# Optimization experiments

Measured on AMD Instinct MI355X. Metric: run time of the kernel, lower is better.

The kernel has to match this reference:

```python
import jax, jax.numpy as jnp
import numpy as np
import math

K_NEIGH = 8
STRIDE = 4
EPS = 1e-8

def _gather(feats, idx):
    # feats (B,N,D), idx (B,M,K) -> (B,M,K,D)
    return jax.vmap(lambda f, i: f[i])(feats, idx)

def _knn_idx(q, p, k):
    # squared-distance KNN, indices sorted by ascending distance
    d2 = (q * q).sum(-1)[:, :, None] + (p * p).sum(-1)[:, None, :] - 2.0 * jnp.einsum('bmd,bnd->bmn', q, p)
    _, idx = jax.lax.top_k(-d2, k)
    return idx

def _fps(pos, k):
    # farthest point sampling, start at index 0 (pytorch3d default)
    B, N, _ = pos.shape
    start = jnp.zeros((B,), dtype=jnp.int32)
    mind = jnp.full((B, N), jnp.inf, dtype=pos.dtype)
    def body(carry, _):
        mind, last = carry
        lp = jax.vmap(lambda p, i: p[i])(pos, last)  # (B,3)
        d = ((pos - lp[:, None, :]) ** 2).sum(-1)
        mind = jnp.minimum(mind, d)
        nxt = jnp.argmax(mind, axis=-1).astype(jnp.int32)
        return (mind, nxt), nxt
    _, nxts = jax.lax.scan(body, (mind, start), None, length=k - 1)
    idx = jnp.concatenate([start[None], nxts], axis=0).swapaxes(0, 1)  # (B,k)
    fp = jax.vmap(lambda p, i: p[i])(pos, idx)
    return fp

def _gelu(t):
    return jax.nn.gelu(t, approximate=False)

def setup_inputs() -> dict:
    key = jax.random.key(0)
    N, B, D = 8192, 2, 128
    ks = jax.random.split(key, 16)
    w = lambda k, i, o: 0.02 * jax.random.normal(k, (i, o), dtype=jnp.float32)
    return {
        'x': jax.random.normal(ks[0], (N, B, D), dtype=jnp.float32),
        'p_pos': jax.random.uniform(ks[1], (B, N, 3), dtype=jnp.float32),
        'Wq': w(ks[2], D, D), 'bq': jnp.zeros((D,), jnp.float32),
        'Wk': w(ks[3], D, D), 'bk': jnp.zeros((D,), jnp.float32),
        'Wv': w(ks[4], D, D), 'bv': jnp.zeros((D,), jnp.float32),
        'Wpe1': w(ks[5], 3, D), 'bpe1': jnp.zeros((D,), jnp.float32),
        'Wpe2': w(ks[6], D, D), 'bpe2': jnp.zeros((D,), jnp.float32),
        'Wg': w(ks[7], D, D), 'bg': jnp.zeros((D,), jnp.float32),
        'Wo': w(ks[8], D, D), 'bo': jnp.zeros((D,), jnp.float32),
        'scale': jnp.ones((D,), jnp.float32),
        'Wf1': w(ks[9], D, 4 * D), 'bf1': jnp.zeros((4 * D,), jnp.float32),
        'Wf2': w(ks[10], 4 * D, 2 * D), 'bf2': jnp.zeros((2 * D,), jnp.float32),
        'Wpool': w(ks[11], 3 + 2 * D, 2 * D),
    }

def reference(x, p_pos, Wq, bq, Wk, bk, Wv, bv, Wpe1, bpe1, Wpe2, bpe2, Wg, bg, Wo, bo, scale, Wf1, bf1, Wf2, bf2, Wpool):
    D = x.shape[-1]
    # --- PointAttention ---
    xt = jnp.swapaxes(x, 0, 1)                      # (B,N,D)
    q = xt @ Wq + bq
    k = xt @ Wk + bk
    v = xt @ Wv + bv
    idx = _knn_idx(p_pos, p_pos, K_NEIGH)           # (B,N,K)
    knn_pos = _gather(p_pos, idx)                   # (B,N,K,3)
    k_knn = _gather(k, idx)
    v_knn = _gather(v, idx)
    pe = _gelu((p_pos[:, :, None, :] - knn_pos) @ Wpe1 + bpe1) @ Wpe2 + bpe2
    attn = (q[:, :, None, :] - k_knn + pe) @ Wg + bg
    attn = jax.nn.softmax(attn / math.sqrt(D), axis=-1)  # softmax over feature dim, as in source
    res = jnp.einsum('bmnf,bmnf->bmf', attn, v_knn + pe)
    res = res @ Wo + bo
    x = x + jnp.swapaxes(res, 0, 1)                 # (N,B,D)
    # --- RMSNorm ---
    rms = jnp.sqrt((x * x).sum(-1, keepdims=True)) / math.sqrt(D)
    x = scale * (x / (rms + EPS))
    # --- FFN ---
    x = _gelu(x @ Wf1 + bf1) @ Wf2 + bf2            # (N,B,2D)
    # --- PointPool ---
    xt2 = jnp.swapaxes(x, 0, 1)                     # (B,N,2D)
    n_out = p_pos.shape[1] // STRIDE
    fp_pos = jax.lax.stop_gradient(_fps(p_pos, n_out))    # (B,n_out,3)
    kidx = jax.lax.stop_gradient(_knn_idx(fp_pos, p_pos, K_NEIGH))
    knn_x = _gather(xt2, kidx)                      # (B,n_out,K,2D)
    h = jnp.concatenate([jnp.broadcast_to(fp_pos[:, :, None, :], knn_x.shape[:3] + (3,)), knn_x], axis=-1)
    h = h @ Wpool
    h = jnp.where(h >= 0, h, 0.01 * h)              # LeakyReLU(0.01)
    h = h.max(axis=-2)                              # (B,n_out,2D)
    return jnp.swapaxes(h, 0, 1), fp_pos
```

## Files before the change

### kernel.cpp

```cpp
#include <hip/hip_runtime.h>
#include <math.h>

#define N_PTS   8192
#define BATCH   2
#define DIM     128
#define NOUT    2048
#define FPOFF   1048576
#define SLICE_MAX 1400

__device__ __forceinline__ float gelu_f(float v) {
  return 0.5f * v * (1.0f + erff(v * 0.70710678118654752440f));
}

__device__ __forceinline__ void knn_insert(float (&dist)[8], int (&idq)[8],
                                           float d2, int ci) {
  if (d2 < dist[7]) {
    float dd = d2;
#pragma unroll
    for (int j = 0; j < 8; ++j) {
      bool cc = dd < dist[j];
      float td = dist[j]; int ti = idq[j];
      dist[j] = cc ? dd : td; idq[j] = cc ? ci : ti;
      dd = cc ? td : dd; ci = cc ? ti : ci;
    }
  }
}

__device__ __forceinline__ void fps_slice(
    const float* __restrict__ P, float* __restrict__ MWS, float* __restrict__ LPWS,
    float* __restrict__ FPWS, float* __restrict__ OUTFP,
    int b, int t0, int t1)
{
  __builtin_amdgcn_s_setprio(3);
  __shared__ unsigned long long wkeys[2][8];
  __shared__ float hist[SLICE_MAX * 3];
  const int tid = threadIdx.x;
  const int wv = tid >> 6;
  const float* __restrict__ Pb = P + (long)b * N_PTS * 3;
  float px[16], py[16], pz[16], mind[16];
#pragma unroll
  for (int s = 0; s < 16; ++s) {
    int i = s * 512 + tid;
    px[s] = Pb[i * 3 + 0];
    py[s] = Pb[i * 3 + 1];
    pz[s] = Pb[i * 3 + 2];
  }
  float lx, ly, lz;
  if (t0 == 0) {
#pragma unroll
    for (int s = 0; s < 16; ++s) mind[s] = INFINITY;
    lx = Pb[0]; ly = Pb[1]; lz = Pb[2];
    if (tid == 0) { hist[0] = lx; hist[1] = ly; hist[2] = lz; }
  } else {
#pragma unroll
    for (int s = 0; s < 16; ++s) mind[s] = MWS[b * N_PTS + s * 512 + tid];
    lx = LPWS[b * 4 + 0]; ly = LPWS[b * 4 + 1]; lz = LPWS[b * 4 + 2];
  }
  const int tstart = (t0 == 0) ? 1 : t0;
  for (int t = tstart; t < t1; ++t) {
    const int par = t & 1;
    float bv = -INFINITY; int bs = 0;
#pragma unroll
    for (int s = 0; s < 16; ++s) {
      float dx = __fsub_rn(px[s], lx);
      float dy = __fsub_rn(py[s], ly);
      float dz = __fsub_rn(pz[s], lz);
      float d = __fadd_rn(__fadd_rn(__fmul_rn(dx, dx), __fmul_rn(dy, dy)), __fmul_rn(dz, dz));
      float mm = fminf(mind[s], d);
      mind[s] = mm;
      bool c = mm > bv;
      bv = c ? mm : bv; bs = c ? s : bs;
    }
    unsigned long long key =
        ((unsigned long long)__float_as_uint(bv) << 32) |
        (unsigned int)~(unsigned int)(bs * 512 + tid);
#pragma unroll
    for (int off = 1; off <= 32; off <<= 1) {
      unsigned long long o = __shfl_xor(key, off);
      key = (o > key) ? o : key;
    }
    if ((tid & 63) == 0) wkeys[par][wv] = key;
    __syncthreads();
    unsigned long long wk = wkeys[par][0];
#pragma unroll
    for (int u = 1; u < 8; ++u) {
      unsigned long long o = wkeys[par][u];
      wk = (o > wk) ? o : wk;
    }
    const int idx = (int)(~(unsigned int)wk);
    lx = Pb[idx * 3 + 0];
    ly = Pb[idx * 3 + 1];
    lz = Pb[idx * 3 + 2];
    if (tid == 0) {
      int h = (t - t0) * 3;
      hist[h + 0] = lx; hist[h + 1] = ly; hist[h + 2] = lz;
    }
  }
#pragma unroll
  for (int s = 0; s < 16; ++s) MWS[b * N_PTS + s * 512 + tid] = mind[s];
  if (tid == 0) { LPWS[b * 4 + 0] = lx; LPWS[b * 4 + 1] = ly; LPWS[b * 4 + 2] = lz; }
  __syncthreads();
  const int cnt = (t1 - t0) * 3;
  const long base = ((long)b * NOUT + t0) * 3;
  for (int i = tid; i < cnt; i += 512) {
    float v2 = hist[i];
    FPWS[base + i] = v2;
    OUTFP[FPOFF + base + i] = v2;
  }
  __builtin_amdgcn_s_setprio(0);
}

__device__ __forceinline__ void knn2p_body(
    const float* __restrict__ Q, const float* __restrict__ Pp,
    float* __restrict__ PD, int* __restrict__ PI, int qg, int r)
{
  __shared__ float4 shp[512];
  const int b = qg >> 2;
  const int m = (qg & 3) * 512 + threadIdx.x;
  const float qx = Q[(b * NOUT + m) * 3 + 0];
  const float qy = Q[(b * NOUT + m) * 3 + 1];
  const float qz = Q[(b * NOUT + m) * 3 + 2];
  const float sqq = __fadd_rn(__fadd_rn(__fmul_rn(qx, qx), __fmul_rn(qy, qy)), __fmul_rn(qz, qz));
  float dist[8]; int idq[8];
#pragma unroll
  for (int j = 0; j < 8; ++j) { dist[j] = INFINITY; idq[j] = 0; }
  const int cb = r * 1024;
  for (int tt = 0; tt < 1024; tt += 512) {
    __syncthreads();
    {
      int l = threadIdx.x;
      float x = Pp[(b * N_PTS + cb + tt + l) * 3 + 0];
      float y = Pp[(b * N_PTS + cb + tt + l) * 3 + 1];
      float z = Pp[(b * N_PTS + cb + tt + l) * 3 + 2];
      float s = __fadd_rn(__fadd_rn(__fmul_rn(x, x), __fmul_rn(y, y)), __fmul_rn(z, z));
      shp[l] = make_float4(x, y, z, s);
    }
    __syncthreads();
    for (int c = 0; c < 512; c += 4) {
      float4 p0 = shp[c + 0];
      float4 p1 = shp[c + 1];
      float4 p2 = shp[c + 2];
      float4 p3 = shp[c + 3];
      float d0 = __fsub_rn(__fadd_rn(sqq, p0.w), __fmul_rn(2.0f,
                 __fadd_rn(__fadd_rn(__fmul_rn(qx, p0.x), __fmul_rn(qy, p0.y)), __fmul_rn(qz, p0.z))));
      float d1 = __fsub_rn(__fadd_rn(sqq, p1.w), __fmul_rn(2.0f,
                 __fadd_rn(__fadd_rn(__fmul_rn(qx, p1.x), __fmul_rn(qy, p1.y)), __fmul_rn(qz, p1.z))));
      float d2 = __fsub_rn(__fadd_rn(sqq, p2.w), __fmul_rn(2.0f,
                 __fadd_rn(__fadd_rn(__fmul_rn(qx, p2.x), __fmul_rn(qy, p2.y)), __fmul_rn(qz, p2.z))));
      float d3 = __fsub_rn(__fadd_rn(sqq, p3.w), __fmul_rn(2.0f,
                 __fadd_rn(__fadd_rn(__fmul_rn(qx, p3.x), __fmul_rn(qy, p3.y)), __fmul_rn(qz, p3.z))));
      float mn = fminf(fminf(d0, d1), fminf(d2, d3));
      if (mn < dist[7]) {
        knn_insert(dist, idq, d0, cb + tt + c + 0);
        knn_insert(dist, idq, d1, cb + tt + c + 1);
        knn_insert(dist, idq, d2, cb + tt + c + 2);
        knn_insert(dist, idq, d3, cb + tt + c + 3);
      }
    }
  }
  const long ob = ((long)(b * NOUT + m) * 8 + r) * 8;
#pragma unroll
  for (int j = 0; j < 8; ++j) { PD[ob + j] = dist[j]; PI[ob + j] = idq[j]; }
}

__global__ __launch_bounds__(512) void fps_fin(
    const float* __restrict__ P, float* __restrict__ MWS, float* __restrict__ LPWS,
    float* __restrict__ FPWS, float* __restrict__ OUTFP,
    float* __restrict__ PD2, int* __restrict__ PI2, int t0, int t1)
{
  if ((int)blockIdx.x < 2) {
    fps_slice(P, MWS, LPWS, FPWS, OUTFP, (int)blockIdx.x, t0, t1);
    return;
  }
  const int wid = (int)blockIdx.x - 2;
  const int qidx = wid >> 3;
  const int r = wid & 7;
  const int qg = qidx * 4;
  knn2p_body(FPWS, P, PD2, PI2, qg, r);
}

__global__ __launch_bounds__(512) void knn2pb_k(
    const float* __restrict__ Q, const float* __restrict__ Pp,
    float* __restrict__ PD, int* __restrict__ PI)
{
  const int qidx = (int)blockIdx.x >> 3;
  const int r = (int)blockIdx.x & 7;
  const int qg = (qidx < 3) ? (qidx + 1) : (qidx + 2);
  knn2p_body(Q, Pp, PD, PI, qg, r);
}

__global__ __launch_bounds__(512) void gemm2_k(
    const float* __restrict__ A, const float* __restrict__ W,
    const float* __restrict__ bias, float* __restrict__ OUT,
    const float* __restrict__ resid,
    int nbx, int N, int K, int a_mode, int o_mode, int act,
    const float* __restrict__ P, float* __restrict__ MWS, float* __restrict__ LPWS,
    float* __restrict__ FPWS, float* __restrict__ OUTFP, int t0, int t1)
{
  if ((int)blockIdx.x < 2) {
    fps_slice(P, MWS, LPWS, FPWS, OUTFP, (int)blockIdx.x, t0, t1);
    return;
  }
  const int wid = (int)blockIdx.x - 2;
  __shared__ float As[2][16][132];
  __shared__ float Ws2[2][16][132];
  const int team = threadIdx.x >> 8;
  const int tid = threadIdx.x & 255;
  const int tx = tid & 15, ty = tid >> 4;
  const int bx = wid % nbx;
  const int byy = (wid / nbx) * 2 + team;
  float acc[8][8];
#pragma unroll
  for (int i = 0; i < 8; ++i)
#pragma unroll
    for (int j = 0; j < 8; ++j) acc[i][j] = 0.f;

  for (int k0 = 0; k0 < K; k0 += 16) {
#pragma unroll
    for (int rep = 0; rep < 2; ++rep) {
      int qq = tid + rep * 256;
      int m = qq >> 2, kq = qq & 3;
      int r = byy * 128 + m;
      int arow = (a_mode == 1) ? ((r & 8191) * 2 + (r >> 13)) : r;
      const float4 av = *(const float4*)(A + (long)arow * K + k0 + kq * 4);
      As[team][kq * 4 + 0][m] = av.x; As[team][kq * 4 + 1][m] = av.y;
      As[team][kq * 4 + 2][m] = av.z; As[team][kq * 4 + 3][m] = av.w;
      int kw = qq >> 5, nq = qq & 31;
      const float4 wv = *(const float4*)(W + (long)(k0 + kw) * N + bx * 128 + nq * 4);
      *(float4*)&Ws2[team][kw][nq * 4] = wv;
    }
    __syncthreads();
#pragma unroll
    for (int kk = 0; kk < 16; ++kk) {
      float4 a0 = *(const float4*)&As[team][kk][ty * 8];
      float4 a1 = *(const float4*)&As[team][kk][ty * 8 + 4];
      float4 w0 = *(const float4*)&Ws2[team][kk][tx * 4];
      float4 w1 = *(const float4*)&Ws2[team][kk][64 + tx * 4];
      float am[8] = {a0.x, a0.y, a0.z, a0.w, a1.x, a1.y, a1.z, a1.w};
      float wn[8] = {w0.x, w0.y, w0.z, w0.w, w1.x, w1.y, w1.z, w1.w};
#pragma unroll
      for (int i = 0; i < 8; ++i)
#pragma unroll
        for (int j = 0; j < 8; ++j) acc[i][j] += am[i] * wn[j];
    }
    __syncthreads();
  }
  const int c0 = bx * 128 + tx * 4;
  const int c1 = c0 + 64;
  float4 ba = *(const float4*)(bias + c0);
  float4 bb = *(const float4*)(bias + c1);
#pragma unroll
  for (int i = 0; i < 8; ++i) {
    int r = byy * 128 + ty * 8 + i;
    int orow = (o_mode == 1) ? ((r & 8191) * 2 + (r >> 13))
             : (o_mode == 2) ? ((r & 1) * 8192 + (r >> 1)) : r;
    float o[8] = {acc[i][0] + ba.x, acc[i][1] + ba.y, acc[i][2] + ba.z, acc[i][3] + ba.w,
                  acc[i][4] + bb.x, acc[i][5] + bb.y, acc[i][6] + bb.z, acc[i][7] + bb.w};
    if (act == 1) {
#pragma unroll
      for (int j = 0; j < 8; ++j) o[j] = gelu_f(o[j]);
    }
    if (resid) {
      float4 r0 = *(const float4*)(resid + (long)orow * N + c0);
      float4 r1 = *(const float4*)(resid + (long)orow * N + c1);
      o[0] += r0.x; o[1] += r0.y; o[2] += r0.z; o[3] += r0.w;
      o[4] += r1.x; o[5] += r1.y; o[6] += r1.z; o[7] += r1.w;
    }
    *(float4*)(OUT + (long)orow * N + c0) = make_float4(o[0], o[1], o[2], o[3]);
    *(float4*)(OUT + (long)orow * N + c1) = make_float4(o[4], o[5], o[6], o[7]);
  }
}

__global__ __launch_bounds__(512) void gemmqkv_k(
    const float* __restrict__ A,
    const float* __restrict__ Wq, const float* __restrict__ bq, float* __restrict__ Oq,
    const float* __restrict__ Wk, const float* __restrict__ bk, float* __restrict__ Ok,
    const float* __restrict__ Wv, const float* __restrict__ bv, float* __restrict__ Ov,
    const float* __restrict__ P, float* __restrict__ MWS, float* __restrict__ LPWS,
    float* __restrict__ FPWS, float* __restrict__ OUTFP, int t0, int t1)
{
  if ((int)blockIdx.x < 2) {
    fps_slice(P, MWS, LPWS, FPWS, OUTFP, (int)blockIdx.x, t0, t1);
    return;
  }
  const int wid = (int)blockIdx.x - 2;
  const int sel = wid >> 6;
  const float* W = (sel == 0) ? Wq : (sel == 1) ? Wk : Wv;
  const float* bias = (sel == 0) ? bq : (sel == 1) ? bk : bv;
  float* OUT = (sel == 0) ? Oq : (sel == 1) ? Ok : Ov;
  __shared__ float As[2][16][132];
  __shared__ float Ws2[2][16][132];
  const int team = threadIdx.x >> 8;
  const int tid = threadIdx.x & 255;
  const int tx = tid & 15, ty = tid >> 4;
  const int byy = (wid & 63) * 2 + team;
  float acc[8][8];
#pragma unroll
  for (int i = 0; i < 8; ++i)
#pragma unroll
    for (int j = 0; j < 8; ++j) acc[i][j] = 0.f;

  for (int k0 = 0; k0 < 128; k0 += 16) {
#pragma unroll
    for (int rep = 0; rep < 2; ++rep) {
      int qq = tid + rep * 256;
      int m = qq >> 2, kq = qq & 3;
      int r = byy * 128 + m;
      int arow = (r & 8191) * 2 + (r >> 13);
      const float4 av = *(const float4*)(A + (long)arow * 128 + k0 + kq * 4);
      As[team][kq * 4 + 0][m] = av.x; As[team][kq * 4 + 1][m] = av.y;
      As[team][kq * 4 + 2][m] = av.z; As[team][kq * 4 + 3][m] = av.w;
      int kw = qq >> 5, nq = qq & 31;
      const float4 wv = *(const float4*)(W + (long)(k0 + kw) * 128 + nq * 4);
      *(float4*)&Ws2[team][kw][nq * 4] = wv;
    }
    __syncthreads();
#pragma unroll
    for (int kk = 0; kk < 16; ++kk) {
      float4 a0 = *(const float4*)&As[team][kk][ty * 8];
      float4 a1 = *(const float4*)&As[team][kk][ty * 8 + 4];
      float4 w0 = *(const float4*)&Ws2[team][kk][tx * 4];
      float4 w1 = *(const float4*)&Ws2[team][kk][64 + tx * 4];
      float am[8] = {a0.x, a0.y, a0.z, a0.w, a1.x, a1.y, a1.z, a1.w};
      float wn[8] = {w0.x, w0.y, w0.z, w0.w, w1.x, w1.y, w1.z, w1.w};
#pragma unroll
      for (int i = 0; i < 8; ++i)
#pragma unroll
        for (int j = 0; j < 8; ++j) acc[i][j] += am[i] * wn[j];
    }
    __syncthreads();
  }
  const int c0 = tx * 4;
  const int c1 = c0 + 64;
  float4 ba = *(const float4*)(bias + c0);
  float4 bb = *(const float4*)(bias + c1);
#pragma unroll
  for (int i = 0; i < 8; ++i) {
    int orow = byy * 128 + ty * 8 + i;
    float o[8] = {acc[i][0] + ba.x, acc[i][1] + ba.y, acc[i][2] + ba.z, acc[i][3] + ba.w,
                  acc[i][4] + bb.x, acc[i][5] + bb.y, acc[i][6] + bb.z, acc[i][7] + bb.w};
    *(float4*)(OUT + (long)orow * 128 + c0) = make_float4(o[0], o[1], o[2], o[3]);
    *(float4*)(OUT + (long)orow * 128 + c1) = make_float4(o[4], o[5], o[6], o[7]);
  }
}

__global__ __launch_bounds__(512) void knn1p_k(
    const float* __restrict__ Pp, float* __restrict__ PD, int* __restrict__ PI,
    const float* __restrict__ P, float* __restrict__ MWS, float* __restrict__ LPWS,
    float* __restrict__ FPWS, float* __restrict__ OUTFP, int t0, int t1)
{
  if ((int)blockIdx.x < 2) {
    fps_slice(P, MWS, LPWS, FPWS, OUTFP, (int)blockIdx.x, t0, t1);
    return;
  }
  const int wid = (int)blockIdx.x - 2;
  const int qg = wid >> 2;
  const int r = wid & 3;
  const int b = qg >> 4;
  const int m = (qg & 15) * 512 + threadIdx.x;
  __shared__ float4 shp[512];
  const float qx = Pp[(b * N_PTS + m) * 3 + 0];
  const float qy = Pp[(b * N_PTS + m) * 3 + 1];
  const float qz = Pp[(b * N_PTS + m) * 3 + 2];
  const float sqq = __fadd_rn(__fadd_rn(__fmul_rn(qx, qx), __fmul_rn(qy, qy)), __fmul_rn(qz, qz));
  float dist[8]; int idq[8];
#pragma unroll
  for (int j = 0; j < 8; ++j) { dist[j] = INFINITY; idq[j] = 0; }
  const int cb = r * 2048;
  for (int tt = 0; tt < 2048; tt += 512) {
    __syncthreads();
    {
      int l = threadIdx.x;
      float x = Pp[(b * N_PTS + cb + tt + l) * 3 + 0];
      float y = Pp[(b * N_PTS + cb + tt + l) * 3 + 1];
      float z = Pp[(b * N_PTS + cb + tt + l) * 3 + 2];
      float s = __fadd_rn(__fadd_rn(__fmul_rn(x, x), __fmul_rn(y, y)), __fmul_rn(z, z));
      shp[l] = make_float4(x, y, z, s);
    }
    __syncthreads();
    for (int c = 0; c < 512; c += 4) {
      float4 p0 = shp[c + 0];
      float4 p1 = shp[c + 1];
      float4 p2 = shp[c + 2];
      float4 p3 = shp[c + 3];
      float d0 = __fsub_rn(__fadd_rn(sqq, p0.w), __fmul_rn(2.0f,
                 __fadd_rn(__fadd_rn(__fmul_rn(qx, p0.x), __fmul_rn(qy, p0.y)), __fmul_rn(qz, p0.z))));
      float d1 = __fsub_rn(__fadd_rn(sqq, p1.w), __fmul_rn(2.0f,
                 __fadd_rn(__fadd_rn(__fmul_rn(qx, p1.x), __fmul_rn(qy, p1.y)), __fmul_rn(qz, p1.z))));
      float d2 = __fsub_rn(__fadd_rn(sqq, p2.w), __fmul_rn(2.0f,
                 __fadd_rn(__fadd_rn(__fmul_rn(qx, p2.x), __fmul_rn(qy, p2.y)), __fmul_rn(qz, p2.z))));
      float d3 = __fsub_rn(__fadd_rn(sqq, p3.w), __fmul_rn(2.0f,
                 __fadd_rn(__fadd_rn(__fmul_rn(qx, p3.x), __fmul_rn(qy, p3.y)), __fmul_rn(qz, p3.z))));
      float mn = fminf(fminf(d0, d1), fminf(d2, d3));
      if (mn < dist[7]) {
        knn_insert(dist, idq, d0, cb + tt + c + 0);
        knn_insert(dist, idq, d1, cb + tt + c + 1);
        knn_insert(dist, idq, d2, cb + tt + c + 2);
        knn_insert(dist, idq, d3, cb + tt + c + 3);
      }
    }
  }
  const long ob = ((long)(b * N_PTS + m) * 4 + r) * 8;
#pragma unroll
  for (int j = 0; j < 8; ++j) { PD[ob + j] = dist[j]; PI[ob + j] = idq[j]; }
}

__global__ __launch_bounds__(512) void attn_k(
    const float* __restrict__ Qb, const float* __restrict__ Kb, const float* __restrict__ Vb,
    const float* __restrict__ Pp,
    const float* __restrict__ PD1, const int* __restrict__ PI1,
    const float* __restrict__ Wpe1, const float* __restrict__ bpe1,
    const float* __restrict__ Wpe2, const float* __restrict__ bpe2,
    const float* __restrict__ Wg, const float* __restrict__ bg,
    float* __restrict__ RES,
    const float* __restrict__ P, float* __restrict__ MWS, float* __restrict__ LPWS,
    float* __restrict__ FPWS, float* __restrict__ OUTFP, int t0, int t1)
{
  if ((int)blockIdx.x < 2) {
    fps_slice(P, MWS, LPWS, FPWS, OUTFP, (int)blockIdx.x, t0, t1);
    return;
  }
  __shared__ float sbuf[8][1024];
  const int tid = threadIdx.x;
  const int w = tid >> 6, lane = tid & 63;
  const int g = ((int)blockIdx.x - 2) * 8 + w;
  const int b = g >> 13, n = g & 8191;
  const int j0 = lane * 2;
  float* sb = sbuf[w];
  const float2 qv = *(const float2*)(Qb + (long)g * 128 + j0);
  float mdist[8]; int nb[8];
#pragma unroll
  for (int j = 0; j < 8; ++j) { mdist[j] = INFINITY; nb[j] = 0; }
#pragma unroll
  for (int r = 0; r < 4; ++r) {
    const long ob = ((long)g * 4 + r) * 8;
#pragma unroll
    for (int j = 0; j < 8; ++j) knn_insert(mdist, nb, PD1[ob + j], PI1[ob + j]);
  }
  const float p0 = Pp[(b * N_PTS + n) * 3 + 0];
  const float p1 = Pp[(b * N_PTS + n) * 3 + 1];
  const float p2 = Pp[(b * N_PTS + n) * 3 + 2];
  const float2 w1a = *(const float2*)(Wpe1 + j0);
  const float2 w1b = *(const float2*)(Wpe1 + 128 + j0);
  const float2 w1c = *(const float2*)(Wpe1 + 256 + j0);
  const float2 b1 = *(const float2*)(bpe1 + j0);
#pragma unroll
  for (int kk = 0; kk < 8; ++kk) {
    const float* pn = Pp + (long)(b * N_PTS + nb[kk]) * 3;
    float r0 = p0 - pn[0], r1 = p1 - pn[1], r2 = p2 - pn[2];
    float h0 = r0 * w1a.x + r1 * w1b.x + r2 * w1c.x + b1.x;
    float h1 = r0 * w1a.y + r1 * w1b.y + r2 * w1c.y + b1.y;
    sb[kk * 128 + j0]     = gelu_f(h0);
    sb[kk * 128 + j0 + 1] = gelu_f(h1);
  }
  __syncthreads();
  float2 pe[8];
#pragma unroll
  for (int kk = 0; kk < 8; ++kk) pe[kk] = make_float2(0.f, 0.f);
  for (int i = 0; i < 128; i += 2) {
    float2 wa = *(const float2*)(Wpe2 + (long)i * 128 + j0);
    float2 wb = *(const float2*)(Wpe2 + (long)(i + 1) * 128 + j0);
#pragma unroll
    for (int kk = 0; kk < 8; ++kk) {
      float2 hh = *(const float2*)&sb[kk * 128 + i];
      pe[kk].x += hh.x * wa.x + hh.y * wb.x;
      pe[kk].y += hh.x * wa.y + hh.y * wb.y;
    }
  }
  const float2 b2v = *(const float2*)(bpe2 + j0);
  __syncthreads();
#pragma unroll
  for (int kk = 0; kk < 8; ++kk) {
    pe[kk].x += b2v.x; pe[kk].y += b2v.y;
    const float2 kv = *(const float2*)(Kb + (long)(b * N_PTS + nb[kk]) * 128 + j0);
    sb[kk * 128 + j0]     = qv.x - kv.x + pe[kk].x;
    sb[kk * 128 + j0 + 1] = qv.y - kv.y + pe[kk].y;
  }
  __syncthreads();
  float2 av[8];
#pragma unroll
  for (int kk = 0; kk < 8; ++kk) av[kk] = make_float2(0.f, 0.f);
  for (int i = 0; i < 128; i += 2) {
    float2 wa = *(const float2*)(Wg + (long)i * 128 + j0);
    float2 wb = *(const float2*)(Wg + (long)(i + 1) * 128 + j0);
#pragma unroll
    for (int kk = 0; kk < 8; ++kk) {
      float2 tt = *(const float2*)&sb[kk * 128 + i];
      av[kk].x += tt.x * wa.x + tt.y * wb.x;
      av[kk].y += tt.x * wa.y + tt.y * wb.y;
    }
  }
  const float2 bgv = *(const float2*)(bg + j0);
  float2 resv = make_float2(0.f, 0.f);
  const float sd = 11.313708498984761f;
#pragma unroll
  for (int kk = 0; kk < 8; ++kk) {
    float l0 = (av[kk].x + bgv.x) / sd;
    float l1 = (av[kk].y + bgv.y) / sd;
    float mx = fmaxf(l0, l1);
#pragma unroll
    for (int off = 32; off >= 1; off >>= 1) mx = fmaxf(mx, __shfl_xor(mx, off));
    float e0 = expf(l0 - mx), e1 = expf(l1 - mx);
    float sm = e0 + e1;
#pragma unroll
    for (int off = 32; off >= 1; off >>= 1) sm += __shfl_xor(sm, off);
    const float2 vv = *(const float2*)(Vb + (long)(b * N_PTS + nb[kk]) * 128 + j0);
    resv.x += (e0 / sm) * (vv.x + pe[kk].x);
    resv.y += (e1 / sm) * (vv.y + pe[kk].y);
  }
  *(float2*)(RES + (long)g * 128 + j0) = resv;
}

__global__ __launch_bounds__(512) void rms_k(
    float* __restrict__ X, const float* __restrict__ scale,
    const float* __restrict__ P, float* __restrict__ MWS, float* __restrict__ LPWS,
    float* __restrict__ FPWS, float* __restrict__ OUTFP, int t0, int t1)
{
  if ((int)blockIdx.x < 2) {
    fps_slice(P, MWS, LPWS, FPWS, OUTFP, (int)blockIdx.x, t0, t1);
    return;
  }
  const int tid = threadIdx.x;
  const int w = tid >> 6, lane = tid & 63;
  const long row = (long)((int)blockIdx.x - 2) * 8 + w;
  float2 xv = *(float2*)(X + row * 128 + lane * 2);
  float ss = xv.x * xv.x + xv.y * xv.y;
#pragma unroll
  for (int off = 32; off >= 1; off >>= 1) ss += __shfl_xor(ss, off);
  const float rms = sqrtf(ss) / 11.313708498984761f;
  const float den = rms + 1e-8f;
  const float2 sc = *(const float2*)(scale + lane * 2);
  float2 o;
  o.x = sc.x * (xv.x / den);
  o.y = sc.y * (xv.y / den);
  *(float2*)(X + row * 128 + lane * 2) = o;
}

__global__ __launch_bounds__(256) void pool_k(
    const float* __restrict__ X3, const float* __restrict__ FPWS,
    const float* __restrict__ PD2, const int* __restrict__ PI2,
    const float* __restrict__ Wp, float* __restrict__ OUT)
{
  __shared__ float sh[8][256];
  __shared__ float fp3[3];
  const int bm = blockIdx.x;
  const int b = bm >> 11;
  const int m = bm & 2047;
  const int tid = threadIdx.x;
  float mdist[8]; int kidx[8];
#pragma unroll
  for (int j = 0; j < 8; ++j) { mdist[j] = INFINITY; kidx[j] = 0; }
#pragma unroll
  for (int r = 0; r < 8; ++r) {
    const long ob = ((long)bm * 8 + r) * 8;
#pragma unroll
    for (int j = 0; j < 8; ++j) knn_insert(mdist, kidx, PD2[ob + j], PI2[ob + j]);
  }
#pragma unroll
  for (int kk = 0; kk < 8; ++kk) {
    sh[kk][tid] = X3[(long)(b * N_PTS + kidx[kk]) * 256 + tid];
  }
  if (tid < 3) fp3[tid] = FPWS[bm * 3 + tid];
  __syncthreads();
  float base = fp3[0] * Wp[tid] + fp3[1] * Wp[256 + tid] + fp3[2] * Wp[512 + tid];
  float acc[8];
#pragma unroll
  for (int kk = 0; kk < 8; ++kk) acc[kk] = base;
  for (int i = 0; i < 256; i += 2) {
    float w0 = Wp[(3 + i) * 256 + tid];
    float w1 = Wp[(4 + i) * 256 + tid];
#pragma unroll
    for (int kk = 0; kk < 8; ++kk) {
      float2 hh = *(const float2*)&sh[kk][i];
      acc[kk] += hh.x * w0 + hh.y * w1;
    }
  }
  float mx = -INFINITY;
#pragma unroll
  for (int kk = 0; kk < 8; ++kk) {
    float a = acc[kk];
    a = (a >= 0.f) ? a : 0.01f * a;
    mx = fmaxf(mx, a);
  }
  OUT[(long)(m * 2 + b) * 256 + tid] = mx;
}

extern "C" void kernel_launch(void* const* d_in, const int* in_sizes, int n_in,
                              void* d_out, int out_size, void* d_ws, size_t ws_size,
                              hipStream_t stream)
{
  (void)in_sizes; (void)n_in; (void)out_size; (void)ws_size;
  const float* x    = (const float*)d_in[0];
  const float* ppos = (const float*)d_in[1];
  const float* Wq = (const float*)d_in[2];   const float* bq = (const float*)d_in[3];
  const float* Wk = (const float*)d_in[4];   const float* bk = (const float*)d_in[5];
  const float* Wv = (const float*)d_in[6];   const float* bv = (const float*)d_in[7];
  const float* Wpe1 = (const float*)d_in[8]; const float* bpe1 = (const float*)d_in[9];
  const float* Wpe2 = (const float*)d_in[10];const float* bpe2 = (const float*)d_in[11];
  const float* Wg = (const float*)d_in[12];  const float* bg = (const float*)d_in[13];
  const float* Wo = (const float*)d_in[14];  const float* bo = (const float*)d_in[15];
  const float* scale = (const float*)d_in[16];
  const float* Wf1 = (const float*)d_in[17]; const float* bf1 = (const float*)d_in[18];
  const float* Wf2 = (const float*)d_in[19]; const float* bf2 = (const float*)d_in[20];
  const float* Wpool = (const float*)d_in[21];
  float* out = (float*)d_out;
  char* ws = (char*)d_ws;

  float* qb   = (float*)(ws);
  float* kb   = (float*)(ws + (size_t)8 * 1024 * 1024);
  float* vb   = (float*)(ws + (size_t)16 * 1024 * 1024);
  float* res  = (float*)(ws + (size_t)24 * 1024 * 1024);
  float* x2   = (float*)(ws + (size_t)32 * 1024 * 1024);
  float* hbuf = (float*)(ws);
  float* x3   = (float*)(ws + (size_t)32 * 1024 * 1024);
  float* PD1  = (float*)(ws + (size_t)32 * 1024 * 1024);
  int*   PI1  = (int*)  (ws + (size_t)34 * 1024 * 1024);
  float* PD2  = (float*)(ws);
  int*   PI2  = (int*)  (ws + (size_t)1 * 1024 * 1024);
  char*  tail = ws + (size_t)48 * 1024 * 1024;
  float* fpws = (float*)(tail);
  float* MWS  = (float*)(tail + 65536);
  float* LPWS = (float*)(tail + 131072);

  gemmqkv_k<<<dim3(194), dim3(512), 0, stream>>>(x, Wq, bq, qb, Wk, bk, kb, Wv, bv, vb,
                                                 ppos, MWS, LPWS, fpws, out, 0, 40);
  knn1p_k<<<dim3(130), dim3(512), 0, stream>>>(ppos, PD1, PI1,
                                               ppos, MWS, LPWS, fpws, out, 40, 100);
  attn_k<<<dim3(2050), dim3(512), 0, stream>>>(qb, kb, vb, ppos, PD1, PI1,
                                               Wpe1, bpe1, Wpe2, bpe2, Wg, bg, res,
                                               ppos, MWS, LPWS, fpws, out, 100, 520);
  gemm2_k<<<dim3(66), dim3(512), 0, stream>>>(res, Wo, bo, x2, x, 1, 128, 128, 0, 1, 0,
                                              ppos, MWS, LPWS, fpws, out, 520, 550);
  rms_k<<<dim3(2050), dim3(512), 0, stream>>>(x2, scale,
                                              ppos, MWS, LPWS, fpws, out, 550, 570);
  gemm2_k<<<dim3(258), dim3(512), 0, stream>>>(x2, Wf1, bf1, hbuf, nullptr, 4, 512, 128, 0, 0, 1,
                                               ppos, MWS, LPWS, fpws, out, 570, 630);
  gemm2_k<<<dim3(130), dim3(512), 0, stream>>>(hbuf, Wf2, bf2, x3, nullptr, 2, 256, 512, 0, 2, 0,
                                               ppos, MWS, LPWS, fpws, out, 630, 670);
  fps_fin<<<dim3(18), dim3(512), 0, stream>>>(ppos, MWS, LPWS, fpws, out, PD2, PI2, 670, 2048);
  knn2pb_k<<<dim3(48), dim3(512), 0, stream>>>(fpws, ppos, PD2, PI2);
  pool_k<<<dim3(4096), dim3(256), 0, stream>>>(x3, fpws, PD2, PI2, Wpool, out);
}
```

Before: 3.220 ms.

## Fuse RMSNorm into Wo GEMM epilogue and rebalance FPS slices across kernels

The separate RMSNorm kernel is removed. Its row reduction now runs in the Wo projection GEMM epilogue, using a 16-lane shuffle across the threads that own one 128-wide row. The farthest-point-sampling iteration ranges carried by the co-running blocks of each kernel are redistributed so that many more FPS steps overlap with the earlier kernels. This leaves fewer serial steps for fps_fin, and SLICE_MAX is lowered to match. The intent is to shorten the FPS tail on the critical path and drop one launch and one activation round trip. The risk is that the longer FPS slices stall the kernels they share a launch with.

```diff
diff --git a/kernel.cpp b/kernel.cpp
--- a/kernel.cpp
+++ b/kernel.cpp
@@ -6,7 +6,7 @@
 #define DIM     128
 #define NOUT    2048
 #define FPOFF   1048576
-#define SLICE_MAX 1400
+#define SLICE_MAX 1000
 
 __device__ __forceinline__ float gelu_f(float v) {
   return 0.5f * v * (1.0f + erff(v * 0.70710678118654752440f));
@@ -192,7 +192,7 @@
 __global__ __launch_bounds__(512) void gemm2_k(
     const float* __restrict__ A, const float* __restrict__ W,
     const float* __restrict__ bias, float* __restrict__ OUT,
-    const float* __restrict__ resid,
+    const float* __restrict__ resid, const float* __restrict__ scale,
     int nbx, int N, int K, int a_mode, int o_mode, int act,
     const float* __restrict__ P, float* __restrict__ MWS, float* __restrict__ LPWS,
     float* __restrict__ FPWS, float* __restrict__ OUTFP, int t0, int t1)
@@ -249,6 +249,11 @@
   const int c1 = c0 + 64;
   float4 ba = *(const float4*)(bias + c0);
   float4 bb = *(const float4*)(bias + c1);
+  float4 sa = make_float4(1.f, 1.f, 1.f, 1.f), sb2 = sa;
+  if (act == 2) {
+    sa  = *(const float4*)(scale + c0);
+    sb2 = *(const float4*)(scale + c1);
+  }
 #pragma unroll
   for (int i = 0; i < 8; ++i) {
     int r = byy * 128 + ty * 8 + i;
@@ -265,6 +270,17 @@
       float4 r1 = *(const float4*)(resid + (long)orow * N + c1);
       o[0] += r0.x; o[1] += r0.y; o[2] += r0.z; o[3] += r0.w;
       o[4] += r1.x; o[5] += r1.y; o[6] += r1.z; o[7] += r1.w;
+    }
+    if (act == 2) {
+      float ss = 0.f;
+#pragma unroll
+      for (int j = 0; j < 8; ++j) ss += o[j] * o[j];
+#pragma unroll
+      for (int off = 1; off <= 8; off <<= 1) ss += __shfl_xor(ss, off);
+      const float den = sqrtf(ss) / 11.313708498984761f + 1e-8f;
+      float sc[8] = {sa.x, sa.y, sa.z, sa.w, sb2.x, sb2.y, sb2.z, sb2.w};
+#pragma unroll
+      for (int j = 0; j < 8; ++j) o[j] = sc[j] * (o[j] / den);
     }
     *(float4*)(OUT + (long)orow * N + c0) = make_float4(o[0], o[1], o[2], o[3]);
     *(float4*)(OUT + (long)orow * N + c1) = make_float4(o[4], o[5], o[6], o[7]);
@@ -511,31 +527,6 @@
   *(float2*)(RES + (long)g * 128 + j0) = resv;
 }
 
-__global__ __launch_bounds__(512) void rms_k(
-    float* __restrict__ X, const float* __restrict__ scale,
-    const float* __restrict__ P, float* __restrict__ MWS, float* __restrict__ LPWS,
-    float* __restrict__ FPWS, float* __restrict__ OUTFP, int t0, int t1)
-{
-  if ((int)blockIdx.x < 2) {
-    fps_slice(P, MWS, LPWS, FPWS, OUTFP, (int)blockIdx.x, t0, t1);
-    return;
-  }
-  const int tid = threadIdx.x;
-  const int w = tid >> 6, lane = tid & 63;
-  const long row = (long)((int)blockIdx.x - 2) * 8 + w;
-  float2 xv = *(float2*)(X + row * 128 + lane * 2);
-  float ss = xv.x * xv.x + xv.y * xv.y;
-#pragma unroll
-  for (int off = 32; off >= 1; off >>= 1) ss += __shfl_xor(ss, off);
-  const float rms = sqrtf(ss) / 11.313708498984761f;
-  const float den = rms + 1e-8f;
-  const float2 sc = *(const float2*)(scale + lane * 2);
-  float2 o;
-  o.x = sc.x * (xv.x / den);
-  o.y = sc.y * (xv.y / den);
-  *(float2*)(X + row * 128 + lane * 2) = o;
-}
-
 __global__ __launch_bounds__(256) void pool_k(
     const float* __restrict__ X3, const float* __restrict__ FPWS,
     const float* __restrict__ PD2, const int* __restrict__ PI2,
@@ -623,21 +614,19 @@
   float* LPWS = (float*)(tail + 131072);
 
   gemmqkv_k<<<dim3(194), dim3(512), 0, stream>>>(x, Wq, bq, qb, Wk, bk, kb, Wv, bv, vb,
-                                                 ppos, MWS, LPWS, fpws, out, 0, 40);
+                                                 ppos, MWS, LPWS, fpws, out, 0, 170);
   knn1p_k<<<dim3(130), dim3(512), 0, stream>>>(ppos, PD1, PI1,
-                                               ppos, MWS, LPWS, fpws, out, 40, 100);
+                                               ppos, MWS, LPWS, fpws, out, 170, 370);
   attn_k<<<dim3(2050), dim3(512), 0, stream>>>(qb, kb, vb, ppos, PD1, PI1,
                                                Wpe1, bpe1, Wpe2, bpe2, Wg, bg, res,
-                                               ppos, MWS, LPWS, fpws, out, 100, 520);
-  gemm2_k<<<dim3(66), dim3(512), 0, stream>>>(res, Wo, bo, x2, x, 1, 128, 128, 0, 1, 0,
-                                              ppos, MWS, LPWS, fpws, out, 520, 550);
-  rms_k<<<dim3(2050), dim3(512), 0, stream>>>(x2, scale,
-                                              ppos, MWS, LPWS, fpws, out, 550, 570);
-  gemm2_k<<<dim3(258), dim3(512), 0, stream>>>(x2, Wf1, bf1, hbuf, nullptr, 4, 512, 128, 0, 0, 1,
-                                               ppos, MWS, LPWS, fpws, out, 570, 630);
-  gemm2_k<<<dim3(130), dim3(512), 0, stream>>>(hbuf, Wf2, bf2, x3, nullptr, 2, 256, 512, 0, 2, 0,
-                                               ppos, MWS, LPWS, fpws, out, 630, 670);
-  fps_fin<<<dim3(18), dim3(512), 0, stream>>>(ppos, MWS, LPWS, fpws, out, PD2, PI2, 670, 2048);
+                                               ppos, MWS, LPWS, fpws, out, 370, 790);
+  gemm2_k<<<dim3(66), dim3(512), 0, stream>>>(res, Wo, bo, x2, x, scale, 1, 128, 128, 0, 1, 2,
+                                              ppos, MWS, LPWS, fpws, out, 790, 860);
+  gemm2_k<<<dim3(258), dim3(512), 0, stream>>>(x2, Wf1, bf1, hbuf, nullptr, nullptr, 4, 512, 128, 0, 0, 1,
+                                               ppos, MWS, LPWS, fpws, out, 860, 1040);
+  gemm2_k<<<dim3(130), dim3(512), 0, stream>>>(hbuf, Wf2, bf2, x3, nullptr, nullptr, 2, 256, 512, 0, 2, 0,
+                                               ppos, MWS, LPWS, fpws, out, 1040, 1130);
+  fps_fin<<<dim3(18), dim3(512), 0, stream>>>(ppos, MWS, LPWS, fpws, out, PD2, PI2, 1130, 2048);
   knn2pb_k<<<dim3(48), dim3(512), 0, stream>>>(fpws, ppos, PD2, PI2);
   pool_k<<<dim3(4096), dim3(256), 0, stream>>>(x3, fpws, PD2, PI2, Wpool, out);
 }
```

Result: faster. 2.986 ms (-7.3%).
